# Kernel optimization log

Measured on AMD Instinct MI355X. Metric: run time of the kernel, lower is better.

## Reference

```python
import jax, jax.numpy as jnp
import numpy as np
from jax import lax

DIM = 768
HEADS = 12
EXPERTS = 4
CAPS = [0.4, 0.3, 0.2, 0.1]  # capacity fraction per expert e=0..E-1 (e=E-1 is the full-dim expert)
EPS = 1e-5


def _layernorm(x, g, b):
    mu = jnp.mean(x, axis=-1, keepdims=True)
    var = jnp.mean(jnp.square(x - mu), axis=-1, keepdims=True)
    return (x - mu) * lax.rsqrt(var + EPS) * g + b


def _route(x, router_w, router_b):
    # Expert-preferred capacity router: experts (largest dim first) greedily take
    # their top-capacity tokens by router probability among still-unassigned tokens.
    B, N, _ = x.shape
    probs = jax.nn.softmax(x @ router_w + router_b, axis=-1)  # [B,N,E]
    ks = [int(c * N) for c in CAPS]
    ks[-1] += N - sum(ks)  # remainder to the largest expert
    assigned = jnp.zeros((B, N), dtype=jnp.int32)
    avail = jnp.ones((B, N), dtype=bool)
    brow = jnp.arange(B)[:, None]
    for e in reversed(range(EXPERTS)):
        pe = jnp.where(avail, probs[:, :, e], -jnp.inf)
        _, idx = lax.top_k(pe, ks[e])  # [B, k_e]
        sel = jnp.zeros((B, N), dtype=bool).at[brow, idx].set(True)
        assigned = jnp.where(sel, e, assigned)
        avail = avail & ~sel
    router_probs = jnp.take_along_axis(probs, assigned[..., None], axis=-1)[..., 0]  # [B,N]
    return assigned, router_probs


def _feat_mask(token_mask, dtype):
    # expert e uses the first DIM / 2^(E-1-e) features (nested slicing)
    dims = jnp.array([DIM >> (EXPERTS - 1 - e) for e in range(EXPERTS)], dtype=jnp.int32)
    d_tok = dims[token_mask]  # [B,N]
    return (jnp.arange(DIM)[None, None, :] < d_tok[..., None]).astype(dtype)  # [B,N,D]


def _nested_attention(h, mask, wqkv, bqkv, wo, bo):
    # masking input + output of a full projection == using the top-left nested submatrix
    B, N, D = h.shape
    hd = D // HEADS
    qkv = ((h * mask) @ wqkv + bqkv) * jnp.tile(mask, (1, 1, 3))  # [B,N,3D]
    q, k, v = jnp.split(qkv, 3, axis=-1)
    q = q.reshape(B, N, HEADS, hd).transpose(0, 2, 1, 3)  # [B,H,N,hd]
    k = k.reshape(B, N, HEADS, hd).transpose(0, 2, 1, 3)
    v = v.reshape(B, N, HEADS, hd).transpose(0, 2, 1, 3)
    scores = jnp.einsum('bhqd,bhkd->bhqk', q, k) * (hd ** -0.5)
    attn = jax.nn.softmax(scores, axis=-1)
    out = jnp.einsum('bhqk,bhkd->bhqd', attn, v)  # [B,H,N,hd]
    out = out.transpose(0, 2, 1, 3).reshape(B, N, D) * mask
    return ((out @ wo) + bo) * mask


def setup_inputs() -> dict:
    key = jax.random.key(0)
    ks = jax.random.split(key, 8)
    B, N, D = 4, 1024, DIM
    s = 0.02
    return {
        'x': jax.random.normal(ks[0], (B, N, D), jnp.float32),
        'ln1_g': jnp.ones((D,), jnp.float32),
        'ln1_b': jnp.zeros((D,), jnp.float32),
        'router_w': jax.random.normal(ks[1], (D, EXPERTS), jnp.float32) * s,
        'router_b': jnp.zeros((EXPERTS,), jnp.float32),
        'wqkv': jax.random.normal(ks[2], (D, 3 * D), jnp.float32) * s,
        'bqkv': jnp.zeros((3 * D,), jnp.float32),
        'wo': jax.random.normal(ks[3], (D, D), jnp.float32) * s,
        'bo': jnp.zeros((D,), jnp.float32),
        'ln2_g': jnp.ones((D,), jnp.float32),
        'ln2_b': jnp.zeros((D,), jnp.float32),
        'w1': jax.random.normal(ks[4], (D, 4 * D), jnp.float32) * s,
        'b1': jnp.zeros((4 * D,), jnp.float32),
        'w2': jax.random.normal(ks[5], (4 * D, D), jnp.float32) * s,
        'b2': jnp.zeros((D,), jnp.float32),
    }


def reference(x, ln1_g, ln1_b, router_w, router_b, wqkv, bqkv, wo, bo,
              ln2_g, ln2_b, w1, b1, w2, b2):
    token_mask, router_probs = _route(x, router_w, router_b)
    mask = _feat_mask(token_mask, x.dtype)  # [B,N,D]
    z = x + _nested_attention(_layernorm(x, ln1_g, ln1_b), mask, wqkv, bqkv, wo, bo)
    h2 = _layernorm(z, ln2_g, ln2_b)
    z_prime = jax.nn.gelu(h2 @ w1 + b1, approximate=False) @ w2 + b2
    # probability-weighted token combine
    return z + router_probs[..., None] * z_prime
```

## Files before the change

kernel.cpp:

```cpp
#include <hip/hip_runtime.h>
#include <math.h>

#define DIM 768
#define NTOK 1024
#define BATCH 4
#define HEADS 12
#define TOKENS (BATCH * NTOK)

typedef __bf16 bf16;
typedef __attribute__((ext_vector_type(8))) __bf16 bf16x8;
typedef __attribute__((ext_vector_type(4))) float floatx4;

__device__ __forceinline__ void async_ld16(const bf16* g, bf16* l) {
    __builtin_amdgcn_global_load_lds((const __attribute__((address_space(1))) unsigned int*)g,
                                     (__attribute__((address_space(3))) unsigned int*)l, 16, 0, 0);
}

__global__ __launch_bounds__(256) void router_kernel(const float* __restrict__ x,
                                                     const float* __restrict__ rw,
                                                     const float* __restrict__ rb,
                                                     float* __restrict__ probs) {
    int t = blockIdx.x * 4 + (threadIdx.x >> 6);
    int lane = threadIdx.x & 63;
    const float* xr = x + (size_t)t * DIM;
    double acc[4] = {0, 0, 0, 0};
#pragma unroll
    for (int i = 0; i < 12; ++i) {
        int k = lane + i * 64;
        double xv = (double)xr[k];
        floatx4 w = *(const floatx4*)&rw[k * 4];
        acc[0] += xv * (double)w[0];
        acc[1] += xv * (double)w[1];
        acc[2] += xv * (double)w[2];
        acc[3] += xv * (double)w[3];
    }
#pragma unroll
    for (int m = 1; m < 64; m <<= 1) {
#pragma unroll
        for (int e = 0; e < 4; ++e) acc[e] += __shfl_xor(acc[e], m);
    }
    if (lane == 0) {
        double lg[4];
        for (int e = 0; e < 4; ++e) lg[e] = acc[e] + (double)rb[e];
        double mx = lg[0];
        for (int e = 1; e < 4; ++e) mx = fmax(mx, lg[e]);
        double s = 0.0, p[4];
        for (int e = 0; e < 4; ++e) { p[e] = exp(lg[e] - mx); s += p[e]; }
        for (int e = 0; e < 4; ++e) probs[(size_t)t * 4 + e] = (float)(p[e] / s);
    }
}

template <int E, int KCAP, bool FIRST, bool LAST>
__global__ __launch_bounds__(256) void route_pass(const float* __restrict__ probs,
                                                  int* __restrict__ avail,
                                                  int* __restrict__ dtok_g,
                                                  float* __restrict__ rprobs_g) {
    int b = blockIdx.y;
    int i = blockIdx.x * 256 + threadIdx.x;
    const float* pb = probs + (size_t)b * NTOK * 4;
    __shared__ float sp[1024];
    for (int j = threadIdx.x; j < 1024; j += 256) {
        bool av = FIRST ? true : (avail[b * NTOK + j] != 0);
        sp[j] = av ? pb[j * 4 + E] : -INFINITY;
    }
    __syncthreads();
    bool av_i = FIRST ? true : (avail[b * NTOK + i] != 0);
    float pi = sp[i];
    int cnt = 0;
#pragma unroll 8
    for (int j0 = 0; j0 < 1024; j0 += 4) {
        floatx4 pj = *(const floatx4*)&sp[j0];
        cnt += (pj[0] > pi) || (pj[0] == pi && (j0 + 0) < i);
        cnt += (pj[1] > pi) || (pj[1] == pi && (j0 + 1) < i);
        cnt += (pj[2] > pi) || (pj[2] == pi && (j0 + 2) < i);
        cnt += (pj[3] > pi) || (pj[3] == pi && (j0 + 3) < i);
    }
    bool sel = av_i && (cnt < KCAP);
    if (sel) {
        dtok_g[b * NTOK + i] = DIM >> (3 - E);
        rprobs_g[b * NTOK + i] = pb[i * 4 + E];
    } else if (LAST && av_i) {
        dtok_g[b * NTOK + i] = DIM >> 3;
        rprobs_g[b * NTOK + i] = pb[i * 4 + 0];
    }
    if (!LAST) {
        if (FIRST) avail[b * NTOK + i] = sel ? 0 : 1;
        else if (sel) avail[b * NTOK + i] = 0;
    }
}

__global__ __launch_bounds__(256) void ln_mask_kernel(const float* __restrict__ x,
                                                      const float* __restrict__ g,
                                                      const float* __restrict__ bta,
                                                      const int* __restrict__ dtok,
                                                      bf16* __restrict__ out) {
    int t = blockIdx.x;
    int tid = threadIdx.x;
    int lane = tid & 63, wv = tid >> 6;
    const float* xr = x + (size_t)t * DIM;
    float v0 = xr[tid], v1 = xr[tid + 256], v2 = xr[tid + 512];
    float s = v0 + v1 + v2;
#pragma unroll
    for (int m = 1; m < 64; m <<= 1) s += __shfl_xor(s, m);
    __shared__ float ws1[4], ws2[4];
    if (lane == 0) ws1[wv] = s;
    __syncthreads();
    float mu = (ws1[0] + ws1[1] + ws1[2] + ws1[3]) * (1.0f / DIM);
    float d0 = v0 - mu, d1 = v1 - mu, d2 = v2 - mu;
    float v = d0 * d0 + d1 * d1 + d2 * d2;
#pragma unroll
    for (int m = 1; m < 64; m <<= 1) v += __shfl_xor(v, m);
    if (lane == 0) ws2[wv] = v;
    __syncthreads();
    float rs = rsqrtf((ws2[0] + ws2[1] + ws2[2] + ws2[3]) * (1.0f / DIM) + 1e-5f);
    int d = dtok ? dtok[t] : DIM;
    out[(size_t)t * DIM + tid] = (bf16)((tid < d) ? d0 * rs * g[tid] + bta[tid] : 0.0f);
    out[(size_t)t * DIM + tid + 256] =
        (bf16)((tid + 256 < d) ? d1 * rs * g[tid + 256] + bta[tid + 256] : 0.0f);
    out[(size_t)t * DIM + tid + 512] =
        (bf16)((tid + 512 < d) ? d2 * rs * g[tid + 512] + bta[tid + 512] : 0.0f);
}

__global__ __launch_bounds__(256) void wo_ln2_kernel(const float* __restrict__ part,
                                                     const float* __restrict__ x,
                                                     const float* __restrict__ bo,
                                                     const int* __restrict__ dtok,
                                                     const float* __restrict__ g,
                                                     const float* __restrict__ bta,
                                                     float* __restrict__ z,
                                                     bf16* __restrict__ h2) {
    int t = blockIdx.x;
    int tid = threadIdx.x;
    int lane = tid & 63, wv = tid >> 6;
    int d = dtok[t];
    float vals[3];
    float s = 0.0f;
#pragma unroll
    for (int i = 0; i < 3; ++i) {
        int k = i * 256 + tid;
        float c = (k < d) ? (part[(size_t)t * DIM + k] +
                             part[(size_t)TOKENS * DIM + (size_t)t * DIM + k] + bo[k])
                          : 0.0f;
        c += x[(size_t)t * DIM + k];
        vals[i] = c;
        s += c;
    }
#pragma unroll
    for (int m = 1; m < 64; m <<= 1) s += __shfl_xor(s, m);
    __shared__ float ws1[4], ws2[4];
    if (lane == 0) ws1[wv] = s;
    __syncthreads();
    float mu = (ws1[0] + ws1[1] + ws1[2] + ws1[3]) * (1.0f / DIM);
    float v = 0.0f;
#pragma unroll
    for (int i = 0; i < 3; ++i) { float dd = vals[i] - mu; v += dd * dd; }
#pragma unroll
    for (int m = 1; m < 64; m <<= 1) v += __shfl_xor(v, m);
    if (lane == 0) ws2[wv] = v;
    __syncthreads();
    float rs = rsqrtf((ws2[0] + ws2[1] + ws2[2] + ws2[3]) * (1.0f / DIM) + 1e-5f);
#pragma unroll
    for (int i = 0; i < 3; ++i) {
        int k = i * 256 + tid;
        z[(size_t)t * DIM + k] = vals[i];
        h2[(size_t)t * DIM + k] = (bf16)((vals[i] - mu) * rs * g[k] + bta[k]);
    }
}

__global__ __launch_bounds__(256) void transpose_all_kernel(const float* __restrict__ wqkv,
                                                            const float* __restrict__ wo,
                                                            const float* __restrict__ w1,
                                                            const float* __restrict__ w2,
                                                            bf16* __restrict__ o0,
                                                            bf16* __restrict__ o1,
                                                            bf16* __restrict__ o2,
                                                            bf16* __restrict__ o3) {
    int id = blockIdx.x;
    const float* W;
    bf16* Wt;
    int K, N, bx, by;
    if (id < 1728) { W = wqkv; Wt = o0; K = 768; N = 2304; bx = id % 72; by = id / 72; }
    else if (id < 2304) { int r = id - 1728; W = wo; Wt = o1; K = 768; N = 768; bx = r % 24; by = r / 24; }
    else if (id < 4608) { int r = id - 2304; W = w1; Wt = o2; K = 768; N = 3072; bx = r % 96; by = r / 96; }
    else { int r = id - 4608; W = w2; Wt = o3; K = 3072; N = 768; bx = r % 24; by = r / 24; }
    __shared__ float t[32][33];
    int x0 = bx * 32, y0 = by * 32;
    int tx = threadIdx.x & 31, ty = threadIdx.x >> 5;
#pragma unroll
    for (int i = 0; i < 4; ++i)
        t[ty + i * 8][tx] = W[(size_t)(y0 + ty + i * 8) * N + x0 + tx];
    __syncthreads();
#pragma unroll
    for (int i = 0; i < 4; ++i)
        Wt[(size_t)(x0 + ty + i * 8) * K + y0 + tx] = (bf16)t[tx][ty + i * 8];
}

__global__ __launch_bounds__(256) void vt_trans_kernel(const bf16* __restrict__ qkv,
                                                       bf16* __restrict__ vtg) {
    int nt = blockIdx.x;
    int h = blockIdx.y;
    int b = blockIdx.z;
    int tid = threadIdx.x;
    __shared__ bf16 T[64 * 72];
    size_t base = (size_t)b * NTOK * 2304;
#pragma unroll
    for (int u = 0; u < 2; ++u) {
        int e = u * 256 + tid;
        int row = e >> 3, part = e & 7;
        *(floatx4*)&T[row * 72 + part * 8] =
            *(const floatx4*)&qkv[base + (size_t)(nt * 64 + row) * 2304 + 1536 + h * 64 + part * 8];
    }
    __syncthreads();
    size_t vbase = ((size_t)(b * HEADS + h)) * 64 * NTOK;
#pragma unroll
    for (int u = 0; u < 2; ++u) {
        int e = u * 256 + tid;
        int d = e >> 3, ng = e & 7;
        bf16 tmp[8];
#pragma unroll
        for (int j = 0; j < 8; ++j) tmp[j] = T[(ng * 8 + j) * 72 + d];
        *(floatx4*)&vtg[vbase + (size_t)d * NTOK + nt * 64 + ng * 8] = *(floatx4*)tmp;
    }
}

template <int MODE>
__global__ __launch_bounds__(256) void gemm_mfma(const bf16* __restrict__ A,
                                                 const bf16* __restrict__ Bt,
                                                 const float* __restrict__ bias,
                                                 void* __restrict__ Cout,
                                                 int M, int NN, int K, int Kc,
                                                 const int* __restrict__ dtok) {
    __shared__ bf16 As[2][64 * 32];
    __shared__ bf16 Bs[2][128 * 32];
    int m0 = blockIdx.x * 64;
    int n0 = blockIdx.y * 128;
    int kbase = blockIdx.z * Kc;
    int tid = threadIdx.x;
    int wv = tid >> 6;
    int lane = tid & 63;
    int l16 = lane & 15, q4 = lane >> 4;
    int wm = (wv >> 1) * 32, wn = (wv & 1) * 64;
    int srow = lane >> 2, scol = (lane & 3) * 8;
    const bf16* gA0 = A + (size_t)(m0 + 16 * wv + srow) * K + kbase + scol;
    const bf16* gB0 = Bt + (size_t)(n0 + 32 * wv + srow) * K + kbase + scol;
    const bf16* gB1 = gB0 + (size_t)16 * K;
    int a0 = (16 * wv) * 32;
    int b0 = (32 * wv) * 32, b1 = (32 * wv + 16) * 32;
    async_ld16(gA0, &As[0][a0]);
    async_ld16(gB0, &Bs[0][b0]);
    async_ld16(gB1, &Bs[0][b1]);
    gA0 += 32; gB0 += 32; gB1 += 32;
    __syncthreads();
    floatx4 acc[2][4] = {};
    int kIters = Kc / 32;
    int cur = 0;
    for (int it = 0; it < kIters; ++it) {
        if (it + 1 < kIters) {
            async_ld16(gA0, &As[cur ^ 1][a0]);
            async_ld16(gB0, &Bs[cur ^ 1][b0]);
            async_ld16(gB1, &Bs[cur ^ 1][b1]);
            gA0 += 32; gB0 += 32; gB1 += 32;
        }
        bf16x8 af[2], bfr[4];
#pragma unroll
        for (int t = 0; t < 2; ++t)
            af[t] = *(const bf16x8*)&As[cur][(wm + t * 16 + l16) * 32 + q4 * 8];
#pragma unroll
        for (int t = 0; t < 4; ++t)
            bfr[t] = *(const bf16x8*)&Bs[cur][(wn + t * 16 + l16) * 32 + q4 * 8];
#pragma unroll
        for (int i = 0; i < 2; ++i)
#pragma unroll
            for (int j = 0; j < 4; ++j)
                acc[i][j] = __builtin_amdgcn_mfma_f32_16x16x32_bf16(af[i], bfr[j], acc[i][j], 0, 0, 0);
        __syncthreads();
        cur ^= 1;
    }
#pragma unroll
    for (int i = 0; i < 2; ++i) {
#pragma unroll
        for (int j = 0; j < 4; ++j) {
            int col = n0 + wn + j * 16 + l16;
#pragma unroll
            for (int r = 0; r < 4; ++r) {
                int row = m0 + wm + i * 16 + q4 * 4 + r;
                if (MODE == 4) {
                    ((float*)Cout)[(size_t)blockIdx.z * M * NN + (size_t)row * NN + col] =
                        acc[i][j][r];
                } else if (MODE == 0) {
                    float c = acc[i][j][r] + bias[col];
                    int jm = col % 768;
                    c = (jm < dtok[row]) ? c : 0.0f;
                    ((bf16*)Cout)[(size_t)row * NN + col] = (bf16)c;
                } else if (MODE == 2) {
                    float c = acc[i][j][r] + bias[col];
                    c = 0.5f * c * (1.0f + erff(c * 0.70710678118654752f));
                    ((bf16*)Cout)[(size_t)row * NN + col] = (bf16)c;
                }
            }
        }
    }
}

__global__ __launch_bounds__(256) void ffn2_reduce(const float* __restrict__ part,
                                                   const float* __restrict__ z,
                                                   const float* __restrict__ bias,
                                                   const float* __restrict__ rp,
                                                   float* __restrict__ out) {
    size_t idx = ((size_t)blockIdx.x * 256 + threadIdx.x) * 4;
    int row = (int)(idx / DIM);
    int col = (int)(idx % DIM);
    floatx4 p0 = *(const floatx4*)&part[idx];
    floatx4 p1 = *(const floatx4*)&part[(size_t)TOKENS * DIM + idx];
    floatx4 zz = *(const floatx4*)&z[idx];
    floatx4 bb = *(const floatx4*)&bias[col];
    float r = rp[row];
    floatx4 o = zz + (p0 + p1 + bb) * r;
    *(floatx4*)&out[idx] = o;
}

#define LDH 72
__global__ __launch_bounds__(256) void attn_mfma(const bf16* __restrict__ qkv,
                                                 const bf16* __restrict__ vtg,
                                                 const int* __restrict__ dtok,
                                                 bf16* __restrict__ attno) {
    int qt = blockIdx.x;
    int h = blockIdx.y;
    int b = blockIdx.z;
    int tid = threadIdx.x;
    int wv = tid >> 6;
    int lane = tid & 63;
    int l16 = lane & 15, q4 = lane >> 4;
    __shared__ bf16 Qs[64 * LDH];
    __shared__ bf16 Ks[64 * LDH];
    __shared__ bf16 Vt[64 * LDH];
    __shared__ bf16 Ps[4][16 * LDH];
    size_t base = (size_t)b * NTOK * 2304;
    size_t vbase = ((size_t)(b * HEADS + h)) * 64 * NTOK;
#pragma unroll
    for (int u = 0; u < 2; ++u) {
        int row = (u * 256 + tid) >> 3, part = (u * 256 + tid) & 7;
        *(floatx4*)&Qs[row * LDH + part * 8] =
            *(const floatx4*)&qkv[base + (size_t)(qt * 64 + row) * 2304 + h * 64 + part * 8];
    }
    floatx4 o[4] = {};
    float psum[4] = {0.0f, 0.0f, 0.0f, 0.0f};
    floatx4 kreg[2], vreg[2];
#pragma unroll
    for (int u = 0; u < 2; ++u) {
        int row = (u * 256 + tid) >> 3, part = (u * 256 + tid) & 7;
        kreg[u] = *(const floatx4*)&qkv[base + (size_t)row * 2304 + 768 + h * 64 + part * 8];
        vreg[u] = *(const floatx4*)&vtg[vbase + (size_t)row * NTOK + part * 8];
    }
    for (int kt = 0; kt < 16; ++kt) {
        __syncthreads();
#pragma unroll
        for (int u = 0; u < 2; ++u) {
            int row = (u * 256 + tid) >> 3, part = (u * 256 + tid) & 7;
            *(floatx4*)&Ks[row * LDH + part * 8] = kreg[u];
            *(floatx4*)&Vt[row * LDH + part * 8] = vreg[u];
        }
        __syncthreads();
        if (kt < 15) {
#pragma unroll
            for (int u = 0; u < 2; ++u) {
                int row = (u * 256 + tid) >> 3, part = (u * 256 + tid) & 7;
                kreg[u] = *(const floatx4*)&qkv[base + (size_t)((kt + 1) * 64 + row) * 2304 + 768 +
                                                h * 64 + part * 8];
                vreg[u] = *(const floatx4*)&vtg[vbase + (size_t)row * NTOK + (kt + 1) * 64 + part * 8];
            }
        }
        floatx4 sc[4] = {};
#pragma unroll
        for (int ch = 0; ch < 2; ++ch) {
            bf16x8 aq = *(const bf16x8*)&Qs[(wv * 16 + l16) * LDH + ch * 32 + q4 * 8];
#pragma unroll
            for (int nt = 0; nt < 4; ++nt) {
                bf16x8 bk = *(const bf16x8*)&Ks[(nt * 16 + l16) * LDH + ch * 32 + q4 * 8];
                sc[nt] = __builtin_amdgcn_mfma_f32_16x16x32_bf16(aq, bk, sc[nt], 0, 0, 0);
            }
        }
#pragma unroll
        for (int nt = 0; nt < 4; ++nt)
#pragma unroll
            for (int r = 0; r < 4; ++r) {
                float p = __expf(sc[nt][r] * 0.125f);
                psum[r] += p;
                Ps[wv][(q4 * 4 + r) * LDH + nt * 16 + l16] = (bf16)p;
            }
#pragma unroll
        for (int ch = 0; ch < 2; ++ch) {
            bf16x8 ap = *(const bf16x8*)&Ps[wv][l16 * LDH + ch * 32 + q4 * 8];
#pragma unroll
            for (int dt = 0; dt < 4; ++dt) {
                bf16x8 bv = *(const bf16x8*)&Vt[(dt * 16 + l16) * LDH + ch * 32 + q4 * 8];
                o[dt] = __builtin_amdgcn_mfma_f32_16x16x32_bf16(ap, bv, o[dt], 0, 0, 0);
            }
        }
    }
#pragma unroll
    for (int r = 0; r < 4; ++r) {
        float s = psum[r];
#pragma unroll
        for (int msk = 1; msk < 16; msk <<= 1) s += __shfl_xor(s, msk);
        int tokrow = qt * 64 + wv * 16 + q4 * 4 + r;
        int dt_tok = dtok[b * NTOK + tokrow];
        float inv = 1.0f / s;
#pragma unroll
        for (int dt = 0; dt < 4; ++dt) {
            int col = h * 64 + dt * 16 + l16;
            float val = (col < dt_tok) ? o[dt][r] * inv : 0.0f;
            attno[((size_t)b * NTOK + tokrow) * DIM + col] = (bf16)val;
        }
    }
}

extern "C" void kernel_launch(void* const* d_in, const int* in_sizes, int n_in,
                              void* d_out, int out_size, void* d_ws, size_t ws_size,
                              hipStream_t stream) {
    const float* x = (const float*)d_in[0];
    const float* ln1g = (const float*)d_in[1];
    const float* ln1b = (const float*)d_in[2];
    const float* rw = (const float*)d_in[3];
    const float* rb = (const float*)d_in[4];
    const float* wqkv = (const float*)d_in[5];
    const float* bqkv = (const float*)d_in[6];
    const float* wo = (const float*)d_in[7];
    const float* bo = (const float*)d_in[8];
    const float* ln2g = (const float*)d_in[9];
    const float* ln2b = (const float*)d_in[10];
    const float* w1 = (const float*)d_in[11];
    const float* b1 = (const float*)d_in[12];
    const float* w2 = (const float*)d_in[13];
    const float* b2 = (const float*)d_in[14];
    float* out = (float*)d_out;

    char* ws = (char*)d_ws;
    size_t off = 0;
    auto alloc = [&](size_t bytes) {
        void* p = ws + off;
        off = (off + bytes + 255) & ~(size_t)255;
        return p;
    };
    bf16* h1m = (bf16*)alloc(sizeof(bf16) * TOKENS * DIM);
    float* probs = (float*)alloc(sizeof(float) * TOKENS * 4);
    float* rprobs = (float*)alloc(sizeof(float) * TOKENS);
    int* dtok = (int*)alloc(sizeof(int) * TOKENS);
    int* avail = (int*)alloc(sizeof(int) * TOKENS);
    bf16* qkvb = (bf16*)alloc(sizeof(bf16) * TOKENS * 3 * DIM);
    bf16* vtg = (bf16*)alloc(sizeof(bf16) * BATCH * HEADS * 64 * NTOK);
    bf16* attno = (bf16*)alloc(sizeof(bf16) * TOKENS * DIM);
    float* z = (float*)alloc(sizeof(float) * TOKENS * DIM);
    bf16* h2 = (bf16*)alloc(sizeof(bf16) * TOKENS * DIM);
    bf16* ffn1 = (bf16*)alloc(sizeof(bf16) * TOKENS * 4 * DIM);
    bf16* wqkvT = (bf16*)alloc(sizeof(bf16) * DIM * 3 * DIM);
    bf16* woT = (bf16*)alloc(sizeof(bf16) * DIM * DIM);
    bf16* w1T = (bf16*)alloc(sizeof(bf16) * DIM * 4 * DIM);
    bf16* w2T = (bf16*)alloc(sizeof(bf16) * 4 * DIM * DIM);
    float* part = (float*)alloc(sizeof(float) * 2 * TOKENS * DIM);

    transpose_all_kernel<<<6912, 256, 0, stream>>>(wqkv, wo, w1, w2, wqkvT, woT, w1T, w2T);

    router_kernel<<<TOKENS / 4, 256, 0, stream>>>(x, rw, rb, probs);
    route_pass<3, 104, true, false><<<dim3(4, BATCH), 256, 0, stream>>>(probs, avail, dtok, rprobs);
    route_pass<2, 204, false, false><<<dim3(4, BATCH), 256, 0, stream>>>(probs, avail, dtok, rprobs);
    route_pass<1, 307, false, true><<<dim3(4, BATCH), 256, 0, stream>>>(probs, avail, dtok, rprobs);
    ln_mask_kernel<<<TOKENS, 256, 0, stream>>>(x, ln1g, ln1b, dtok, h1m);
    gemm_mfma<0><<<dim3(4096 / 64, 2304 / 128), 256, 0, stream>>>(
        h1m, wqkvT, bqkv, qkvb, TOKENS, 2304, 768, 768, dtok);
    vt_trans_kernel<<<dim3(16, HEADS, BATCH), 256, 0, stream>>>(qkvb, vtg);
    attn_mfma<<<dim3(16, HEADS, BATCH), 256, 0, stream>>>(qkvb, vtg, dtok, attno);
    gemm_mfma<4><<<dim3(4096 / 64, 768 / 128, 2), 256, 0, stream>>>(
        attno, woT, nullptr, part, TOKENS, 768, 768, 384, nullptr);
    wo_ln2_kernel<<<TOKENS, 256, 0, stream>>>(part, x, bo, dtok, ln2g, ln2b, z, h2);
    gemm_mfma<2><<<dim3(4096 / 64, 3072 / 128), 256, 0, stream>>>(
        h2, w1T, b1, ffn1, TOKENS, 3072, 768, 768, nullptr);
    gemm_mfma<4><<<dim3(4096 / 64, 768 / 128, 2), 256, 0, stream>>>(
        ffn1, w2T, nullptr, part, TOKENS, 768, 3072, 1536, nullptr);
    ffn2_reduce<<<TOKENS * DIM / 1024, 256, 0, stream>>>(part, z, b2, rprobs, out);
}
```

Before: 396.7 us.

## Fuse epilogues into GEMMs, drop split-K, swizzle LDS, merge prep kernels

Merges the router and weight-transpose kernels into one launch. Writes V transposed directly from the QKV GEMM epilogue, removing the separate vt_trans kernel. Drops split-K for the Wo and FFN2 GEMMs and fuses the residual/bias/router-weighted combine into their epilogues, eliminating the fp32 partial buffers and two reduce kernels. It also adds an XOR swizzle to the LDS tile layout to reduce bank conflicts. The trade-off is fewer blocks for the K=3072 GEMM, plus uncoalesced scattered stores for the V transpose.

After: 406.5 us. 1.02x slower.

```diff
diff --git a/kernel.cpp b/kernel.cpp
--- a/kernel.cpp
+++ b/kernel.cpp
@@ -16,38 +16,65 @@
                                      (__attribute__((address_space(3))) unsigned int*)l, 16, 0, 0);
 }
 
-__global__ __launch_bounds__(256) void router_kernel(const float* __restrict__ x,
-                                                     const float* __restrict__ rw,
-                                                     const float* __restrict__ rb,
-                                                     float* __restrict__ probs) {
-    int t = blockIdx.x * 4 + (threadIdx.x >> 6);
-    int lane = threadIdx.x & 63;
-    const float* xr = x + (size_t)t * DIM;
-    double acc[4] = {0, 0, 0, 0};
-#pragma unroll
-    for (int i = 0; i < 12; ++i) {
-        int k = lane + i * 64;
-        double xv = (double)xr[k];
-        floatx4 w = *(const floatx4*)&rw[k * 4];
-        acc[0] += xv * (double)w[0];
-        acc[1] += xv * (double)w[1];
-        acc[2] += xv * (double)w[2];
-        acc[3] += xv * (double)w[3];
-    }
-#pragma unroll
-    for (int m = 1; m < 64; m <<= 1) {
-#pragma unroll
-        for (int e = 0; e < 4; ++e) acc[e] += __shfl_xor(acc[e], m);
-    }
-    if (lane == 0) {
-        double lg[4];
-        for (int e = 0; e < 4; ++e) lg[e] = acc[e] + (double)rb[e];
-        double mx = lg[0];
-        for (int e = 1; e < 4; ++e) mx = fmax(mx, lg[e]);
-        double s = 0.0, p[4];
-        for (int e = 0; e < 4; ++e) { p[e] = exp(lg[e] - mx); s += p[e]; }
-        for (int e = 0; e < 4; ++e) probs[(size_t)t * 4 + e] = (float)(p[e] / s);
-    }
+__global__ __launch_bounds__(256) void prep_kernel(const float* __restrict__ wqkv,
+                                                   const float* __restrict__ wo,
+                                                   const float* __restrict__ w1,
+                                                   const float* __restrict__ w2,
+                                                   bf16* __restrict__ o0, bf16* __restrict__ o1,
+                                                   bf16* __restrict__ o2, bf16* __restrict__ o3,
+                                                   const float* __restrict__ x,
+                                                   const float* __restrict__ rw,
+                                                   const float* __restrict__ rb,
+                                                   float* __restrict__ probs) {
+    int id = blockIdx.x;
+    if (id >= 6912) {
+        int t = (id - 6912) * 4 + (threadIdx.x >> 6);
+        int lane = threadIdx.x & 63;
+        const float* xr = x + (size_t)t * DIM;
+        double acc[4] = {0, 0, 0, 0};
+#pragma unroll
+        for (int i = 0; i < 12; ++i) {
+            int k = lane + i * 64;
+            double xv = (double)xr[k];
+            floatx4 w = *(const floatx4*)&rw[k * 4];
+            acc[0] += xv * (double)w[0];
+            acc[1] += xv * (double)w[1];
+            acc[2] += xv * (double)w[2];
+            acc[3] += xv * (double)w[3];
+        }
+#pragma unroll
+        for (int m = 1; m < 64; m <<= 1) {
+#pragma unroll
+            for (int e = 0; e < 4; ++e) acc[e] += __shfl_xor(acc[e], m);
+        }
+        if (lane == 0) {
+            double lg[4];
+            for (int e = 0; e < 4; ++e) lg[e] = acc[e] + (double)rb[e];
+            double mx = lg[0];
+            for (int e = 1; e < 4; ++e) mx = fmax(mx, lg[e]);
+            double s = 0.0, p[4];
+            for (int e = 0; e < 4; ++e) { p[e] = exp(lg[e] - mx); s += p[e]; }
+            for (int e = 0; e < 4; ++e) probs[(size_t)t * 4 + e] = (float)(p[e] / s);
+        }
+        return;
+    }
+    const float* W;
+    bf16* Wt;
+    int K, N, bx, by;
+    if (id < 1728) { W = wqkv; Wt = o0; K = 768; N = 2304; bx = id % 72; by = id / 72; }
+    else if (id < 2304) { int r = id - 1728; W = wo; Wt = o1; K = 768; N = 768; bx = r % 24; by = r / 24; }
+    else if (id < 4608) { int r = id - 2304; W = w1; Wt = o2; K = 768; N = 3072; bx = r % 96; by = r / 96; }
+    else { int r = id - 4608; W = w2; Wt = o3; K = 3072; N = 768; bx = r % 24; by = r / 24; }
+    __shared__ float t[32][33];
+    int x0 = bx * 32, y0 = by * 32;
+    int tx = threadIdx.x & 31, ty = threadIdx.x >> 5;
+#pragma unroll
+    for (int i = 0; i < 4; ++i)
+        t[ty + i * 8][tx] = W[(size_t)(y0 + ty + i * 8) * N + x0 + tx];
+    __syncthreads();
+#pragma unroll
+    for (int i = 0; i < 4; ++i)
+        Wt[(size_t)(x0 + ty + i * 8) * K + y0 + tx] = (bf16)t[tx][ty + i * 8];
 }
 
 template <int E, int KCAP, bool FIRST, bool LAST>
@@ -121,128 +148,29 @@
         (bf16)((tid + 512 < d) ? d2 * rs * g[tid + 512] + bta[tid + 512] : 0.0f);
 }
 
-__global__ __launch_bounds__(256) void wo_ln2_kernel(const float* __restrict__ part,
-                                                     const float* __restrict__ x,
-                                                     const float* __restrict__ bo,
-                                                     const int* __restrict__ dtok,
-                                                     const float* __restrict__ g,
-                                                     const float* __restrict__ bta,
-                                                     float* __restrict__ z,
-                                                     bf16* __restrict__ h2) {
-    int t = blockIdx.x;
-    int tid = threadIdx.x;
-    int lane = tid & 63, wv = tid >> 6;
-    int d = dtok[t];
-    float vals[3];
-    float s = 0.0f;
-#pragma unroll
-    for (int i = 0; i < 3; ++i) {
-        int k = i * 256 + tid;
-        float c = (k < d) ? (part[(size_t)t * DIM + k] +
-                             part[(size_t)TOKENS * DIM + (size_t)t * DIM + k] + bo[k])
-                          : 0.0f;
-        c += x[(size_t)t * DIM + k];
-        vals[i] = c;
-        s += c;
-    }
-#pragma unroll
-    for (int m = 1; m < 64; m <<= 1) s += __shfl_xor(s, m);
-    __shared__ float ws1[4], ws2[4];
-    if (lane == 0) ws1[wv] = s;
-    __syncthreads();
-    float mu = (ws1[0] + ws1[1] + ws1[2] + ws1[3]) * (1.0f / DIM);
-    float v = 0.0f;
-#pragma unroll
-    for (int i = 0; i < 3; ++i) { float dd = vals[i] - mu; v += dd * dd; }
-#pragma unroll
-    for (int m = 1; m < 64; m <<= 1) v += __shfl_xor(v, m);
-    if (lane == 0) ws2[wv] = v;
-    __syncthreads();
-    float rs = rsqrtf((ws2[0] + ws2[1] + ws2[2] + ws2[3]) * (1.0f / DIM) + 1e-5f);
-#pragma unroll
-    for (int i = 0; i < 3; ++i) {
-        int k = i * 256 + tid;
-        z[(size_t)t * DIM + k] = vals[i];
-        h2[(size_t)t * DIM + k] = (bf16)((vals[i] - mu) * rs * g[k] + bta[k]);
-    }
-}
-
-__global__ __launch_bounds__(256) void transpose_all_kernel(const float* __restrict__ wqkv,
-                                                            const float* __restrict__ wo,
-                                                            const float* __restrict__ w1,
-                                                            const float* __restrict__ w2,
-                                                            bf16* __restrict__ o0,
-                                                            bf16* __restrict__ o1,
-                                                            bf16* __restrict__ o2,
-                                                            bf16* __restrict__ o3) {
-    int id = blockIdx.x;
-    const float* W;
-    bf16* Wt;
-    int K, N, bx, by;
-    if (id < 1728) { W = wqkv; Wt = o0; K = 768; N = 2304; bx = id % 72; by = id / 72; }
-    else if (id < 2304) { int r = id - 1728; W = wo; Wt = o1; K = 768; N = 768; bx = r % 24; by = r / 24; }
-    else if (id < 4608) { int r = id - 2304; W = w1; Wt = o2; K = 768; N = 3072; bx = r % 96; by = r / 96; }
-    else { int r = id - 4608; W = w2; Wt = o3; K = 3072; N = 768; bx = r % 24; by = r / 24; }
-    __shared__ float t[32][33];
-    int x0 = bx * 32, y0 = by * 32;
-    int tx = threadIdx.x & 31, ty = threadIdx.x >> 5;
-#pragma unroll
-    for (int i = 0; i < 4; ++i)
-        t[ty + i * 8][tx] = W[(size_t)(y0 + ty + i * 8) * N + x0 + tx];
-    __syncthreads();
-#pragma unroll
-    for (int i = 0; i < 4; ++i)
-        Wt[(size_t)(x0 + ty + i * 8) * K + y0 + tx] = (bf16)t[tx][ty + i * 8];
-}
-
-__global__ __launch_bounds__(256) void vt_trans_kernel(const bf16* __restrict__ qkv,
-                                                       bf16* __restrict__ vtg) {
-    int nt = blockIdx.x;
-    int h = blockIdx.y;
-    int b = blockIdx.z;
-    int tid = threadIdx.x;
-    __shared__ bf16 T[64 * 72];
-    size_t base = (size_t)b * NTOK * 2304;
-#pragma unroll
-    for (int u = 0; u < 2; ++u) {
-        int e = u * 256 + tid;
-        int row = e >> 3, part = e & 7;
-        *(floatx4*)&T[row * 72 + part * 8] =
-            *(const floatx4*)&qkv[base + (size_t)(nt * 64 + row) * 2304 + 1536 + h * 64 + part * 8];
-    }
-    __syncthreads();
-    size_t vbase = ((size_t)(b * HEADS + h)) * 64 * NTOK;
-#pragma unroll
-    for (int u = 0; u < 2; ++u) {
-        int e = u * 256 + tid;
-        int d = e >> 3, ng = e & 7;
-        bf16 tmp[8];
-#pragma unroll
-        for (int j = 0; j < 8; ++j) tmp[j] = T[(ng * 8 + j) * 72 + d];
-        *(floatx4*)&vtg[vbase + (size_t)d * NTOK + nt * 64 + ng * 8] = *(floatx4*)tmp;
-    }
-}
-
 template <int MODE>
 __global__ __launch_bounds__(256) void gemm_mfma(const bf16* __restrict__ A,
                                                  const bf16* __restrict__ Bt,
                                                  const float* __restrict__ bias,
                                                  void* __restrict__ Cout,
-                                                 int M, int NN, int K, int Kc,
-                                                 const int* __restrict__ dtok) {
+                                                 int M, int NN, int K,
+                                                 const int* __restrict__ dtok,
+                                                 const float* __restrict__ aux,
+                                                 const float* __restrict__ rp,
+                                                 bf16* __restrict__ vtg) {
     __shared__ bf16 As[2][64 * 32];
     __shared__ bf16 Bs[2][128 * 32];
     int m0 = blockIdx.x * 64;
     int n0 = blockIdx.y * 128;
-    int kbase = blockIdx.z * Kc;
     int tid = threadIdx.x;
     int wv = tid >> 6;
     int lane = tid & 63;
     int l16 = lane & 15, q4 = lane >> 4;
     int wm = (wv >> 1) * 32, wn = (wv & 1) * 64;
-    int srow = lane >> 2, scol = (lane & 3) * 8;
-    const bf16* gA0 = A + (size_t)(m0 + 16 * wv + srow) * K + kbase + scol;
-    const bf16* gB0 = Bt + (size_t)(n0 + 32 * wv + srow) * K + kbase + scol;
+    int srow = lane >> 2;
+    int scol = (((lane & 3) ^ (srow & 3)) * 8);
+    const bf16* gA0 = A + (size_t)(m0 + 16 * wv + srow) * K + scol;
+    const bf16* gB0 = Bt + (size_t)(n0 + 32 * wv + srow) * K + scol;
     const bf16* gB1 = gB0 + (size_t)16 * K;
     int a0 = (16 * wv) * 32;
     int b0 = (32 * wv) * 32, b1 = (32 * wv + 16) * 32;
@@ -252,8 +180,9 @@
     gA0 += 32; gB0 += 32; gB1 += 32;
     __syncthreads();
     floatx4 acc[2][4] = {};
-    int kIters = Kc / 32;
+    int kIters = K / 32;
     int cur = 0;
+    bool vb = (MODE == 0) && (n0 >= 1536);
     for (int it = 0; it < kIters; ++it) {
         if (it + 1 < kIters) {
             async_ld16(gA0, &As[cur ^ 1][a0]);
@@ -261,21 +190,53 @@
             async_ld16(gB1, &Bs[cur ^ 1][b1]);
             gA0 += 32; gB0 += 32; gB1 += 32;
         }
+        int gsl = (q4 ^ (l16 & 3)) * 8;
         bf16x8 af[2], bfr[4];
 #pragma unroll
         for (int t = 0; t < 2; ++t)
-            af[t] = *(const bf16x8*)&As[cur][(wm + t * 16 + l16) * 32 + q4 * 8];
+            af[t] = *(const bf16x8*)&As[cur][(wm + t * 16 + l16) * 32 + gsl];
 #pragma unroll
         for (int t = 0; t < 4; ++t)
-            bfr[t] = *(const bf16x8*)&Bs[cur][(wn + t * 16 + l16) * 32 + q4 * 8];
-#pragma unroll
-        for (int i = 0; i < 2; ++i)
-#pragma unroll
-            for (int j = 0; j < 4; ++j)
-                acc[i][j] = __builtin_amdgcn_mfma_f32_16x16x32_bf16(af[i], bfr[j], acc[i][j], 0, 0, 0);
+            bfr[t] = *(const bf16x8*)&Bs[cur][(wn + t * 16 + l16) * 32 + gsl];
+        if (vb) {
+#pragma unroll
+            for (int i = 0; i < 2; ++i)
+#pragma unroll
+                for (int j = 0; j < 4; ++j)
+                    acc[i][j] =
+                        __builtin_amdgcn_mfma_f32_16x16x32_bf16(bfr[j], af[i], acc[i][j], 0, 0, 0);
+        } else {
+#pragma unroll
+            for (int i = 0; i < 2; ++i)
+#pragma unroll
+                for (int j = 0; j < 4; ++j)
+                    acc[i][j] =
+                        __builtin_amdgcn_mfma_f32_16x16x32_bf16(af[i], bfr[j], acc[i][j], 0, 0, 0);
+        }
         __syncthreads();
         cur ^= 1;
     }
+    if (MODE == 0 && n0 >= 1536) {
+#pragma unroll
+        for (int i = 0; i < 2; ++i) {
+            int tok = m0 + wm + i * 16 + l16;
+            int dt_tok = dtok[tok];
+            int b = tok >> 10, n = tok & 1023;
+#pragma unroll
+            for (int j = 0; j < 4; ++j) {
+#pragma unroll
+                for (int r = 0; r < 4; ++r) {
+                    int col = n0 + wn + j * 16 + q4 * 4 + r;
+                    int vcol = col - 1536;
+                    float c = acc[i][j][r] + bias[col];
+                    c = (vcol < dt_tok) ? c : 0.0f;
+                    int h = vcol >> 6, d = vcol & 63;
+                    vtg[(size_t)((b * HEADS + h) * 64 + d) * NTOK + n] = (bf16)c;
+                }
+            }
+        }
+        return;
+    }
 #pragma unroll
     for (int i = 0; i < 2; ++i) {
 #pragma unroll
@@ -284,39 +245,28 @@
 #pragma unroll
             for (int r = 0; r < 4; ++r) {
                 int row = m0 + wm + i * 16 + q4 * 4 + r;
-                if (MODE == 4) {
-                    ((float*)Cout)[(size_t)blockIdx.z * M * NN + (size_t)row * NN + col] =
-                        acc[i][j][r];
-                } else if (MODE == 0) {
+                if (MODE == 0) {
                     float c = acc[i][j][r] + bias[col];
                     int jm = col % 768;
                     c = (jm < dtok[row]) ? c : 0.0f;
                     ((bf16*)Cout)[(size_t)row * NN + col] = (bf16)c;
+                } else if (MODE == 1) {
+                    float c = acc[i][j][r] + bias[col];
+                    c = (col < dtok[row]) ? c : 0.0f;
+                    c += aux[(size_t)row * DIM + col];
+                    ((float*)Cout)[(size_t)row * NN + col] = c;
                 } else if (MODE == 2) {
                     float c = acc[i][j][r] + bias[col];
                     c = 0.5f * c * (1.0f + erff(c * 0.70710678118654752f));
                     ((bf16*)Cout)[(size_t)row * NN + col] = (bf16)c;
+                } else {
+                    float c = acc[i][j][r] + bias[col];
+                    ((float*)Cout)[(size_t)row * NN + col] =
+                        aux[(size_t)row * DIM + col] + rp[row] * c;
                 }
             }
         }
     }
-}
-
-__global__ __launch_bounds__(256) void ffn2_reduce(const float* __restrict__ part,
-                                                   const float* __restrict__ z,
-                                                   const float* __restrict__ bias,
-                                                   const float* __restrict__ rp,
-                                                   float* __restrict__ out) {
-    size_t idx = ((size_t)blockIdx.x * 256 + threadIdx.x) * 4;
-    int row = (int)(idx / DIM);
-    int col = (int)(idx % DIM);
-    floatx4 p0 = *(const floatx4*)&part[idx];
-    floatx4 p1 = *(const floatx4*)&part[(size_t)TOKENS * DIM + idx];
-    floatx4 zz = *(const floatx4*)&z[idx];
-    floatx4 bb = *(const floatx4*)&bias[col];
-    float r = rp[row];
-    floatx4 o = zz + (p0 + p1 + bb) * r;
-    *(floatx4*)&out[idx] = o;
 }
 
 #define LDH 72
@@ -457,25 +407,21 @@
     bf16* woT = (bf16*)alloc(sizeof(bf16) * DIM * DIM);
     bf16* w1T = (bf16*)alloc(sizeof(bf16) * DIM * 4 * DIM);
     bf16* w2T = (bf16*)alloc(sizeof(bf16) * 4 * DIM * DIM);
-    float* part = (float*)alloc(sizeof(float) * 2 * TOKENS * DIM);
-
-    transpose_all_kernel<<<6912, 256, 0, stream>>>(wqkv, wo, w1, w2, wqkvT, woT, w1T, w2T);
-
-    router_kernel<<<TOKENS / 4, 256, 0, stream>>>(x, rw, rb, probs);
+
+    prep_kernel<<<6912 + TOKENS / 4, 256, 0, stream>>>(wqkv, wo, w1, w2, wqkvT, woT, w1T, w2T,
+                                                       x, rw, rb, probs);
     route_pass<3, 104, true, false><<<dim3(4, BATCH), 256, 0, stream>>>(probs, avail, dtok, rprobs);
     route_pass<2, 204, false, false><<<dim3(4, BATCH), 256, 0, stream>>>(probs, avail, dtok, rprobs);
     route_pass<1, 307, false, true><<<dim3(4, BATCH), 256, 0, stream>>>(probs, avail, dtok, rprobs);
     ln_mask_kernel<<<TOKENS, 256, 0, stream>>>(x, ln1g, ln1b, dtok, h1m);
     gemm_mfma<0><<<dim3(4096 / 64, 2304 / 128), 256, 0, stream>>>(
-        h1m, wqkvT, bqkv, qkvb, TOKENS, 2304, 768, 768, dtok);
-    vt_trans_kernel<<<dim3(16, HEADS, BATCH), 256, 0, stream>>>(qkvb, vtg);
+        h1m, wqkvT, bqkv, qkvb, TOKENS, 2304, 768, dtok, nullptr, nullptr, vtg);
     attn_mfma<<<dim3(16, HEADS, BATCH), 256, 0, stream>>>(qkvb, vtg, dtok, attno);
-    gemm_mfma<4><<<dim3(4096 / 64, 768 / 128, 2), 256, 0, stream>>>(
-        attno, woT, nullptr, part, TOKENS, 768, 768, 384, nullptr);
-    wo_ln2_kernel<<<TOKENS, 256, 0, stream>>>(part, x, bo, dtok, ln2g, ln2b, z, h2);
+    gemm_mfma<1><<<dim3(4096 / 64, 768 / 128), 256, 0, stream>>>(
+        attno, woT, bo, z, TOKENS, 768, 768, dtok, x, nullptr, nullptr);
+    ln_mask_kernel<<<TOKENS, 256, 0, stream>>>(z, ln2g, ln2b, nullptr, h2);
     gemm_mfma<2><<<dim3(4096 / 64, 3072 / 128), 256, 0, stream>>>(
-        h2, w1T, b1, ffn1, TOKENS, 3072, 768, 768, nullptr);
-    gemm_mfma<4><<<dim3(4096 / 64, 768 / 128, 2), 256, 0, stream>>>(
-        ffn1, w2T, nullptr, part, TOKENS, 768, 3072, 1536, nullptr);
-    ffn2_reduce<<<TOKENS * DIM / 1024, 256, 0, stream>>>(part, z, b2, rprobs, out);
-}
+        h2, w1T, b1, ffn1, TOKENS, 3072, 768, nullptr, nullptr, nullptr, nullptr);
+    gemm_mfma<3><<<dim3(4096 / 64, 768 / 128), 256, 0, stream>>>(
+        ffn1, w2T, b2, out, TOKENS, 768, 3072, nullptr, z, rprobs, nullptr);
+}
```
